# Kernel optimization log

Hardware: AMD Instinct MI355X
Metric: run time of the kernel (lower is better)

The kernel has to match this reference:

```python
import jax, jax.numpy as jnp
import numpy as np

DIM = 1024
NUM_HEADS = 16
DIM_PER_HEAD = 64
INNER = NUM_HEADS * DIM_PER_HEAD  # 1024
SCALE = DIM_PER_HEAD ** -0.5
EPS = 1e-10


def setup_inputs() -> dict:
    key = jax.random.key(0)
    k_x, k_m, k_qkv, k_wo, k_bo = jax.random.split(key, 5)
    b, l = 2, 2048
    x = jax.random.normal(k_x, (b, l, DIM), dtype=jnp.float32)
    # binary multiplicative mask [b, l, l]
    mask = jax.random.randint(k_m, (b, l, l), 0, 2).astype(jnp.float32)
    # nn.Linear(dim, 3*inner, bias=False): weight [3*inner, dim]; we store transposed [dim, 3*inner]
    W_qkv = jax.random.normal(k_qkv, (DIM, 3 * INNER), dtype=jnp.float32) * (DIM ** -0.5)
    W_out = jax.random.normal(k_wo, (INNER, DIM), dtype=jnp.float32) * (INNER ** -0.5)
    b_out = jax.random.normal(k_bo, (DIM,), dtype=jnp.float32) * 0.01
    return {"x": x, "mask": mask, "W_qkv": W_qkv, "W_out": W_out, "b_out": b_out}


def reference(x, mask, W_qkv, W_out, b_out):
    b, l, d = x.shape
    qkv = x @ W_qkv  # [b, l, 3*inner]
    qkv = qkv.reshape(b, l, 3, NUM_HEADS, DIM_PER_HEAD)
    qkv = jnp.transpose(qkv, (2, 0, 3, 1, 4))  # [3, b, h, l, dh]
    q, k, v = qkv[0], qkv[1], qkv[2]
    # softmax FIRST (no additive mask), matching the original module
    attn = jax.nn.softmax(jnp.einsum('bhid,bhjd->bhij', q, k) * SCALE, axis=-1)  # [b,h,l,l]
    # multiplicative mask then renormalize
    attn = attn * mask[:, None, :, :]
    attn = attn / (jnp.sum(attn, axis=-1, keepdims=True) + EPS)
    z = jnp.einsum('bhij,bhjd->bhid', attn, v)  # [b,h,l,dh]
    z = jnp.transpose(z, (0, 2, 1, 3)).reshape(b, l, INNER)
    out = z @ W_out + b_out  # dropout p=0 -> identity
    return out
```

## Files before the change

kernel.cpp:

```cpp
#include <hip/hip_runtime.h>
#include <hip/hip_bf16.h>

#define BATCH 2
#define SEQ   2048
#define DIM   1024
#define HEADS 16
#define DH    64
#define N_QKV 3072
#define M_TOT 4096
#define SCALE 0.125f
#define EPS   1e-10f
#define LOG2E 1.442695041f

typedef __attribute__((ext_vector_type(8))) _Float16 half8;
typedef __attribute__((ext_vector_type(4))) float f32x4;

static __device__ __forceinline__ unsigned short f2h(float f) {
    _Float16 h = (_Float16)f;
    return __builtin_bit_cast(unsigned short, h);
}
static __device__ __forceinline__ unsigned int pkrtz(float a, float b) {
#if defined(__has_builtin) && __has_builtin(__builtin_amdgcn_cvt_pkrtz)
    return __builtin_bit_cast(unsigned int, __builtin_amdgcn_cvt_pkrtz(a, b));
#else
    return (unsigned int)f2h(a) | ((unsigned int)f2h(b) << 16);
#endif
}
static __device__ __forceinline__ void glds16(const void* g, void* l) {
    __builtin_amdgcn_global_load_lds((const __attribute__((address_space(1))) void*)g,
                                     (__attribute__((address_space(3))) void*)l,
                                     16, 0, 0);
}

__global__ __launch_bounds__(256) void prepass(const float* __restrict__ x,
                                               unsigned short* __restrict__ xh,
                                               const float* __restrict__ Wq,
                                               unsigned short* __restrict__ WqT,
                                               const float* __restrict__ Wo,
                                               unsigned short* __restrict__ WoT,
                                               const float* __restrict__ mask,
                                               unsigned short* __restrict__ mbits) {
    const int bid = blockIdx.x;
    const int t   = threadIdx.x;
    __shared__ float tile[32][33];
    __shared__ unsigned char flags[16][256];

    if (bid < 4096) {
        const int i = bid * 256 + t;
        float4 v = reinterpret_cast<const float4*>(x)[i];
        uint2 o;
        o.x = pkrtz(v.x, v.y);
        o.y = pkrtz(v.z, v.w);
        reinterpret_cast<uint2*>(xh)[i] = o;
    } else if (bid < 8192) {
        const float* src; unsigned short* th; int rows, cols, bx;
        if (bid < 7168) { src = Wq; th = WqT; rows = 1024; cols = 3072; bx = bid - 4096;
        } else          { src = Wo; th = WoT; rows = 1024; cols = 1024; bx = bid - 7168; }
        const int nbx = cols / 32;
        const int c0 = (bx % nbx) * 32, r0 = (bx / nbx) * 32;
        const int tx = t & 31, ty = t >> 5;
        #pragma unroll
        for (int i = ty; i < 32; i += 8)
            tile[i][tx] = src[(long)(r0 + i) * cols + c0 + tx];
        __syncthreads();
        #pragma unroll
        for (int i = ty; i < 32; i += 8)
            th[(long)(c0 + i) * rows + r0 + tx] = f2h(tile[tx][i]);
    } else {
        const int bx = bid - 8192;
        const int it = bx & 127;
        const int bb = bx >> 7;
        const int R0 = it * 16;
        const int tl = t >> 6, ln = t & 63;
        for (int c0 = 0; c0 < SEQ; c0 += 256) {
            #pragma unroll
            for (int rr = 0; rr < 16; ++rr)
                flags[rr][t] = mask[((long)bb * SEQ + R0 + rr) * SEQ + c0 + t] != 0.f;
            __syncthreads();
            unsigned int bits = 0;
            #pragma unroll
            for (int nt = 0; nt < 4; ++nt)
                #pragma unroll
                for (int r = 0; r < 4; ++r)
                    bits |= (unsigned int)flags[ln & 15][tl * 64 + nt * 16 + ((ln >> 4) << 2) + r]
                            << (nt * 4 + r);
            mbits[(((long)bb * 128 + it) * 32 + (c0 >> 6) + tl) * 64 + ln] = (unsigned short)bits;
            __syncthreads();
        }
    }
}

__global__ __launch_bounds__(256, 3) void gemm_qkv_f16(
    const unsigned short* __restrict__ Ahg, const unsigned short* __restrict__ Bhg,
    unsigned short* __restrict__ qb, unsigned short* __restrict__ kb,
    unsigned short* __restrict__ vtb) {
    __shared__ __align__(16) unsigned short As[128 * 64];
    __shared__ __align__(16) unsigned short Bs[128 * 64];

    const int n0   = blockIdx.x * 128;
    const int m0   = blockIdx.y * 128;
    const int wave = threadIdx.x >> 6;
    const int lane = threadIdx.x & 63;
    const int l16  = lane & 15;
    const int g    = lane >> 4;
    const int wm   = wave & 1;
    const int wn   = wave >> 1;
    const int sw   = l16 & 7;

    const int sr8 = lane >> 3;
    const int scg = (lane & 7) ^ sr8;

    f32x4 acc[4][4] = {};

    for (int k0 = 0; k0 < DIM; k0 += 64) {
        #pragma unroll
        for (int i = 0; i < 4; ++i) {
            const int row = wave * 32 + i * 8;
            glds16(Ahg + (long)(m0 + row + sr8) * DIM + k0 + scg * 8, &As[row * 64]);
            glds16(Bhg + (long)(n0 + row + sr8) * DIM + k0 + scg * 8, &Bs[row * 64]);
        }
        __syncthreads();

        #pragma unroll
        for (int kc = 0; kc < 2; ++kc) {
            half8 a[4], b[4];
            #pragma unroll
            for (int mt = 0; mt < 4; ++mt)
                a[mt] = *reinterpret_cast<const half8*>(
                    &As[(wm * 64 + mt * 16 + l16) * 64 + (((kc * 4 + g) ^ sw) * 8)]);
            #pragma unroll
            for (int nt = 0; nt < 4; ++nt)
                b[nt] = *reinterpret_cast<const half8*>(
                    &Bs[(wn * 64 + nt * 16 + l16) * 64 + (((kc * 4 + g) ^ sw) * 8)]);
            #pragma unroll
            for (int mt = 0; mt < 4; ++mt)
                #pragma unroll
                for (int nt = 0; nt < 4; ++nt)
                    acc[mt][nt] = __builtin_amdgcn_mfma_f32_16x16x32_f16(
                        a[mt], b[nt], acc[mt][nt], 0, 0, 0);
        }
        __syncthreads();
    }

    #pragma unroll
    for (int nt = 0; nt < 4; ++nt) {
        const int n     = n0 + wn * 64 + nt * 16 + l16;
        const int which = n >> 10;
        const int rem   = n & 1023;
        const int head  = rem >> 6;
        const int d     = rem & 63;
        #pragma unroll
        for (int mt = 0; mt < 4; ++mt) {
            #pragma unroll
            for (int r = 0; r < 4; ++r) {
                const int m  = m0 + wm * 64 + mt * 16 + g * 4 + r;
                const int bb = m >> 11;
                const int li = m & 2047;
                const int bh_i = bb * HEADS + head;
                const float val = acc[mt][nt][r];
                if (which == 0)
                    qb[((long)bh_i * SEQ + li) * DH + d] = f2h(val * (SCALE * LOG2E));
                else if (which == 1)
                    kb[((long)bh_i * SEQ + li) * DH + d] = f2h(val);
                else
                    vtb[((long)bh_i * DH + d) * SEQ + li] = f2h(val);
            }
        }
    }
}

__global__ __launch_bounds__(256, 4) void gemm_out_f16(
    const unsigned short* __restrict__ Ahg, const unsigned short* __restrict__ Bhg,
    const float* __restrict__ bias, float* __restrict__ out) {
    __shared__ __align__(16) unsigned short As[64 * 64];
    __shared__ __align__(16) unsigned short Bs[64 * 64];

    const int n0   = blockIdx.x * 64;
    const int m0   = blockIdx.y * 64;
    const int wave = threadIdx.x >> 6;
    const int lane = threadIdx.x & 63;
    const int l16  = lane & 15;
    const int g    = lane >> 4;
    const int wm   = wave & 1;
    const int wn   = wave >> 1;
    const int sw   = l16 & 7;

    const int sr8 = lane >> 3;
    const int scg = (lane & 7) ^ sr8;

    f32x4 acc[2][2] = {};

    for (int k0 = 0; k0 < DIM; k0 += 64) {
        #pragma unroll
        for (int i = 0; i < 2; ++i) {
            const int row = wave * 16 + i * 8;
            glds16(Ahg + (long)(m0 + row + sr8) * DIM + k0 + scg * 8, &As[row * 64]);
            glds16(Bhg + (long)(n0 + row + sr8) * DIM + k0 + scg * 8, &Bs[row * 64]);
        }
        __syncthreads();

        half8 a[2][2];
        #pragma unroll
        for (int mt = 0; mt < 2; ++mt) {
            const int rbase = (wm * 32 + mt * 16 + l16) * 64;
            #pragma unroll
            for (int kc = 0; kc < 2; ++kc)
                a[mt][kc] = *reinterpret_cast<const half8*>(
                    &As[rbase + (((kc * 4 + g) ^ sw) * 8)]);
        }
        #pragma unroll
        for (int nt = 0; nt < 2; ++nt) {
            const int rbase = (wn * 32 + nt * 16 + l16) * 64;
            const half8 b0 = *reinterpret_cast<const half8*>(&Bs[rbase + (((0 + g) ^ sw) * 8)]);
            const half8 b1 = *reinterpret_cast<const half8*>(&Bs[rbase + (((4 + g) ^ sw) * 8)]);
            #pragma unroll
            for (int mt = 0; mt < 2; ++mt) {
                acc[mt][nt] = __builtin_amdgcn_mfma_f32_16x16x32_f16(a[mt][0], b0, acc[mt][nt], 0, 0, 0);
                acc[mt][nt] = __builtin_amdgcn_mfma_f32_16x16x32_f16(a[mt][1], b1, acc[mt][nt], 0, 0, 0);
            }
        }
        __syncthreads();
    }

    #pragma unroll
    for (int nt = 0; nt < 2; ++nt) {
        const int n  = n0 + wn * 32 + nt * 16 + l16;
        const float bv = bias[n];
        #pragma unroll
        for (int mt = 0; mt < 2; ++mt) {
            #pragma unroll
            for (int r = 0; r < 4; ++r) {
                const int m = m0 + wm * 32 + mt * 16 + g * 4 + r;
                out[(long)m * DIM + n] = acc[mt][nt][r] + bv;
            }
        }
    }
}

__global__ __launch_bounds__(512, 4) void attn_mfma(const unsigned short* __restrict__ qb,
                                                    const unsigned short* __restrict__ kb,
                                                    const unsigned short* __restrict__ vtb,
                                                    const unsigned short* __restrict__ mbits,
                                                    unsigned short* __restrict__ zh) {
    const int qt   = blockIdx.x;
    const int h    = blockIdx.y;
    const int bb   = blockIdx.z;
    const int bh   = bb * HEADS + h;
    const int wave = threadIdx.x >> 6;
    const int lane = threadIdx.x & 63;
    const int l16  = lane & 15;
    const int g    = lane >> 4;
    const int wm   = wave >> 1;
    const int wj   = wave & 1;

    const int myrow0 = qt * 128 + wm * 32;

    __shared__ __align__(16) unsigned short shm[32768];

    const int sr8 = lane >> 3;
    const int scg = (lane & 7) ^ sr8;
    const int sw  = l16 & 7;

    unsigned short* Ks = &shm[wj * 8192];
    unsigned short* Vs = &shm[wj * 8192 + 4096];
    unsigned short* P0 = &shm[16384 + wave * 1024];
    unsigned short* P1 = &shm[24576 + wave * 1024];

    const unsigned short* qptr = qb + ((long)bh * SEQ + myrow0 + l16) * DH + g * 8;
    const half8 q0 = *reinterpret_cast<const half8*>(qptr);
    const half8 q1 = *reinterpret_cast<const half8*>(qptr + 32);
    const half8 q2 = *reinterpret_cast<const half8*>(qptr + 16 * DH);
    const half8 q3 = *reinterpret_cast<const half8*>(qptr + 16 * DH + 32);

    half8 ones;
    #pragma unroll
    for (int j = 0; j < 8; ++j) ones[j] = (_Float16)1.0f;

    f32x4 o0[4] = {}, o1[4] = {};
    f32x4 oz0 = {0.f, 0.f, 0.f, 0.f};
    f32x4 oz1 = {0.f, 0.f, 0.f, 0.f};

    const unsigned short* mb =
        mbits + (((long)bb * 128 + qt * 8 + wm * 2) * 32 + wj * 16) * 64 + lane;
    const long kbase = (long)bh * SEQ * DH;
    const long vbase = (long)bh * DH * SEQ;
    const int  jb    = wj * 1024;

    for (int it = 0; it < 16; ++it) {
        const int j0 = jb + it * 64;
        const unsigned int bits0 = mb[(long)it * 64];
        const unsigned int bits1 = mb[(long)it * 64 + 2048];

        #pragma unroll
        for (int i = 0; i < 2; ++i) {
            const int row = wm * 16 + i * 8;
            glds16(kb  + kbase + (long)(j0 + row + sr8) * DH + scg * 8, Ks + row * 64);
            glds16(vtb + vbase + (long)(row + sr8) * SEQ + j0 + scg * 8, Vs + row * 64);
        }
        __syncthreads();

        #pragma unroll
        for (int nt = 0; nt < 4; ++nt) {
            const int rbase = (nt * 16 + l16) * 64;
            const half8 k0 = *reinterpret_cast<const half8*>(&Ks[rbase + ((0 + g) ^ sw) * 8]);
            const half8 k1 = *reinterpret_cast<const half8*>(&Ks[rbase + (((4 + g) ^ sw) * 8)]);
            f32x4 s0 = {0.f, 0.f, 0.f, 0.f};
            f32x4 s1 = {0.f, 0.f, 0.f, 0.f};
            s0 = __builtin_amdgcn_mfma_f32_16x16x32_f16(k0, q0, s0, 0, 0, 0);
            s0 = __builtin_amdgcn_mfma_f32_16x16x32_f16(k1, q1, s0, 0, 0, 0);
            s1 = __builtin_amdgcn_mfma_f32_16x16x32_f16(k0, q2, s1, 0, 0, 0);
            s1 = __builtin_amdgcn_mfma_f32_16x16x32_f16(k1, q3, s1, 0, 0, 0);

            float pa[4], pb[4];
            #pragma unroll
            for (int r = 0; r < 4; ++r) {
                const float e0 = __builtin_amdgcn_exp2f(s0[r]);
                const float e1 = __builtin_amdgcn_exp2f(s1[r]);
                pa[r] = ((bits0 >> (nt * 4 + r)) & 1u) ? e0 : 0.f;
                pb[r] = ((bits1 >> (nt * 4 + r)) & 1u) ? e1 : 0.f;
            }
            const int poff = l16 * 64 + (((2 * nt + (g >> 1)) ^ sw) * 8) + (g & 1) * 4;
            uint2 pk0, pk1;
            pk0.x = pkrtz(pa[0], pa[1]);
            pk0.y = pkrtz(pa[2], pa[3]);
            pk1.x = pkrtz(pb[0], pb[1]);
            pk1.y = pkrtz(pb[2], pb[3]);
            *reinterpret_cast<uint2*>(&P0[poff]) = pk0;
            *reinterpret_cast<uint2*>(&P1[poff]) = pk1;
        }

        const half8 pb00 = *reinterpret_cast<const half8*>(&P0[l16 * 64 + ((0 + g) ^ sw) * 8]);
        const half8 pb01 = *reinterpret_cast<const half8*>(&P0[l16 * 64 + (((4 + g) ^ sw) * 8)]);
        const half8 pb10 = *reinterpret_cast<const half8*>(&P1[l16 * 64 + ((0 + g) ^ sw) * 8]);
        const half8 pb11 = *reinterpret_cast<const half8*>(&P1[l16 * 64 + (((4 + g) ^ sw) * 8)]);

        #pragma unroll
        for (int dt = 0; dt < 4; ++dt) {
            const int vb = (dt * 16 + l16) * 64;
            const half8 v0 = *reinterpret_cast<const half8*>(&Vs[vb + ((0 + g) ^ sw) * 8]);
            const half8 v1 = *reinterpret_cast<const half8*>(&Vs[vb + (((4 + g) ^ sw) * 8)]);
            o0[dt] = __builtin_amdgcn_mfma_f32_16x16x32_f16(v0, pb00, o0[dt], 0, 0, 0);
            o0[dt] = __builtin_amdgcn_mfma_f32_16x16x32_f16(v1, pb01, o0[dt], 0, 0, 0);
            o1[dt] = __builtin_amdgcn_mfma_f32_16x16x32_f16(v0, pb10, o1[dt], 0, 0, 0);
            o1[dt] = __builtin_amdgcn_mfma_f32_16x16x32_f16(v1, pb11, o1[dt], 0, 0, 0);
        }
        oz0 = __builtin_amdgcn_mfma_f32_16x16x32_f16(ones, pb00, oz0, 0, 0, 0);
        oz0 = __builtin_amdgcn_mfma_f32_16x16x32_f16(ones, pb01, oz0, 0, 0, 0);
        oz1 = __builtin_amdgcn_mfma_f32_16x16x32_f16(ones, pb10, oz1, 0, 0, 0);
        oz1 = __builtin_amdgcn_mfma_f32_16x16x32_f16(ones, pb11, oz1, 0, 0, 0);
        __syncthreads();
    }

    float* cmb = (float*)shm;
    const int ZOFF = 128 * 68;
    const int ci0  = wm * 32 + l16;
    const int ci1  = ci0 + 16;
    if (wj == 1) {
        #pragma unroll
        for (int dt = 0; dt < 4; ++dt) {
            *reinterpret_cast<f32x4*>(&cmb[ci0 * 68 + dt * 16 + g * 4]) = o0[dt];
            *reinterpret_cast<f32x4*>(&cmb[ci1 * 68 + dt * 16 + g * 4]) = o1[dt];
        }
        if (g == 0) {
            cmb[ZOFF + ci0] = oz0[0];
            cmb[ZOFF + ci1] = oz1[0];
        }
    }
    __syncthreads();
    if (wj == 0) {
        const float Z0   = oz0[0] + cmb[ZOFF + ci0];
        const float Z1   = oz1[0] + cmb[ZOFF + ci1];
        const float inv0 = 1.f / (Z0 + 1e-30f);
        const float inv1 = 1.f / (Z1 + 1e-30f);
        const long obase0 = ((long)bb * SEQ + myrow0 + l16) * DIM + h * DH;
        const long obase1 = obase0 + (long)16 * DIM;
        #pragma unroll
        for (int dt = 0; dt < 4; ++dt) {
            const f32x4 oc0 = *reinterpret_cast<const f32x4*>(&cmb[ci0 * 68 + dt * 16 + g * 4]);
            const f32x4 oc1 = *reinterpret_cast<const f32x4*>(&cmb[ci1 * 68 + dt * 16 + g * 4]);
            uint2 pk;
            pk.x = pkrtz((o0[dt][0] + oc0[0]) * inv0, (o0[dt][1] + oc0[1]) * inv0);
            pk.y = pkrtz((o0[dt][2] + oc0[2]) * inv0, (o0[dt][3] + oc0[3]) * inv0);
            *reinterpret_cast<uint2*>(zh + obase0 + dt * 16 + g * 4) = pk;
            pk.x = pkrtz((o1[dt][0] + oc1[0]) * inv1, (o1[dt][1] + oc1[1]) * inv1);
            pk.y = pkrtz((o1[dt][2] + oc1[2]) * inv1, (o1[dt][3] + oc1[3]) * inv1);
            *reinterpret_cast<uint2*>(zh + obase1 + dt * 16 + g * 4) = pk;
        }
    }
}

extern "C" void kernel_launch(void* const* d_in, const int* in_sizes, int n_in,
                              void* d_out, int out_size, void* d_ws, size_t ws_size,
                              hipStream_t stream) {
    const float* x     = (const float*)d_in[0];
    const float* mask  = (const float*)d_in[1];
    const float* W_qkv = (const float*)d_in[2];
    const float* W_out = (const float*)d_in[3];
    const float* b_out = (const float*)d_in[4];
    float* out = (float*)d_out;

    unsigned short* ws = (unsigned short*)d_ws;
    unsigned short* xh    = ws;
    unsigned short* WqT   = xh    + 4194304;
    unsigned short* WoT   = WqT   + 3145728;
    unsigned short* qbu   = WoT   + 1048576;
    unsigned short* kbu   = qbu   + 4194304;
    unsigned short* vtb   = kbu   + 4194304;
    unsigned short* mbits = vtb   + 4194304;
    unsigned short* zz    = xh;

    prepass<<<8448, 256, 0, stream>>>(x, xh, W_qkv, WqT, W_out, WoT, mask, mbits);

    gemm_qkv_f16<<<dim3(24, 32), 256, 0, stream>>>(xh, WqT, qbu, kbu, vtb);

    attn_mfma<<<dim3(SEQ / 128, HEADS, BATCH), 512, 0, stream>>>(qbu, kbu, vtb, mbits, zz);

    gemm_out_f16<<<dim3(16, 64), 256, 0, stream>>>(zz, WoT, b_out, out);
}
```

Baseline: 229.9 us.

## Halve attention block to 64 query rows with XCD-aware flat grid and shared P buffer

```diff
diff --git a/kernel.cpp b/kernel.cpp
--- a/kernel.cpp
+++ b/kernel.cpp
@@ -237,14 +237,18 @@
     }
 }
 
-__global__ __launch_bounds__(512, 4) void attn_mfma(const unsigned short* __restrict__ qb,
+__global__ __launch_bounds__(256, 4) void attn_mfma(const unsigned short* __restrict__ qb,
                                                     const unsigned short* __restrict__ kb,
                                                     const unsigned short* __restrict__ vtb,
                                                     const unsigned short* __restrict__ mbits,
                                                     unsigned short* __restrict__ zh) {
-    const int qt   = blockIdx.x;
-    const int h    = blockIdx.y;
-    const int bb   = blockIdx.z;
+    const int flat = blockIdx.x;
+    const int xcd  = flat & 7;
+    const int rr   = flat >> 3;
+    const int hh   = xcd + 8 * (rr >> 5);
+    const int qt   = rr & 31;
+    const int h    = hh & 15;
+    const int bb   = hh >> 4;
     const int bh   = bb * HEADS + h;
     const int wave = threadIdx.x >> 6;
     const int lane = threadIdx.x & 63;
@@ -253,18 +257,16 @@
     const int wm   = wave >> 1;
     const int wj   = wave & 1;
 
-    const int myrow0 = qt * 128 + wm * 32;
-
-    __shared__ __align__(16) unsigned short shm[32768];
+    const int myrow0 = qt * 64 + wm * 32;
+
+    __shared__ __align__(16) unsigned short shm[20480];
+    unsigned short* Ks = &shm[wj * 8192];
+    unsigned short* Vs = &shm[wj * 8192 + 4096];
+    unsigned short* Pw = &shm[16384 + wave * 1024];
 
     const int sr8 = lane >> 3;
     const int scg = (lane & 7) ^ sr8;
     const int sw  = l16 & 7;
-
-    unsigned short* Ks = &shm[wj * 8192];
-    unsigned short* Vs = &shm[wj * 8192 + 4096];
-    unsigned short* P0 = &shm[16384 + wave * 1024];
-    unsigned short* P1 = &shm[24576 + wave * 1024];
 
     const unsigned short* qptr = qb + ((long)bh * SEQ + myrow0 + l16) * DH + g * 8;
     const half8 q0 = *reinterpret_cast<const half8*>(qptr);
@@ -281,24 +283,24 @@
     f32x4 oz1 = {0.f, 0.f, 0.f, 0.f};
 
     const unsigned short* mb =
-        mbits + (((long)bb * 128 + qt * 8 + wm * 2) * 32 + wj * 16) * 64 + lane;
+        mbits + (((long)bb * 128 + qt * 4 + wm * 2) * 32 + wj * 16) * 64 + lane;
     const long kbase = (long)bh * SEQ * DH;
     const long vbase = (long)bh * DH * SEQ;
-    const int  jb    = wj * 1024;
 
     for (int it = 0; it < 16; ++it) {
-        const int j0 = jb + it * 64;
+        const int j0 = wj * 1024 + it * 64;
         const unsigned int bits0 = mb[(long)it * 64];
         const unsigned int bits1 = mb[(long)it * 64 + 2048];
 
         #pragma unroll
-        for (int i = 0; i < 2; ++i) {
-            const int row = wm * 16 + i * 8;
+        for (int i = 0; i < 4; ++i) {
+            const int row = wm * 32 + i * 8;
             glds16(kb  + kbase + (long)(j0 + row + sr8) * DH + scg * 8, Ks + row * 64);
             glds16(vtb + vbase + (long)(row + sr8) * SEQ + j0 + scg * 8, Vs + row * 64);
         }
         __syncthreads();
 
+        uint2 p1s[4];
         #pragma unroll
         for (int nt = 0; nt < 4; ++nt) {
             const int rbase = (nt * 16 + l16) * 64;
@@ -320,19 +322,23 @@
                 pb[r] = ((bits1 >> (nt * 4 + r)) & 1u) ? e1 : 0.f;
             }
             const int poff = l16 * 64 + (((2 * nt + (g >> 1)) ^ sw) * 8) + (g & 1) * 4;
-            uint2 pk0, pk1;
+            uint2 pk0;
             pk0.x = pkrtz(pa[0], pa[1]);
             pk0.y = pkrtz(pa[2], pa[3]);
-            pk1.x = pkrtz(pb[0], pb[1]);
-            pk1.y = pkrtz(pb[2], pb[3]);
-            *reinterpret_cast<uint2*>(&P0[poff]) = pk0;
-            *reinterpret_cast<uint2*>(&P1[poff]) = pk1;
-        }
-
-        const half8 pb00 = *reinterpret_cast<const half8*>(&P0[l16 * 64 + ((0 + g) ^ sw) * 8]);
-        const half8 pb01 = *reinterpret_cast<const half8*>(&P0[l16 * 64 + (((4 + g) ^ sw) * 8)]);
-        const half8 pb10 = *reinterpret_cast<const half8*>(&P1[l16 * 64 + ((0 + g) ^ sw) * 8]);
-        const half8 pb11 = *reinterpret_cast<const half8*>(&P1[l16 * 64 + (((4 + g) ^ sw) * 8)]);
+            *reinterpret_cast<uint2*>(&Pw[poff]) = pk0;
+            p1s[nt].x = pkrtz(pb[0], pb[1]);
+            p1s[nt].y = pkrtz(pb[2], pb[3]);
+        }
+
+        const half8 pb00 = *reinterpret_cast<const half8*>(&Pw[l16 * 64 + ((0 + g) ^ sw) * 8]);
+        const half8 pb01 = *reinterpret_cast<const half8*>(&Pw[l16 * 64 + (((4 + g) ^ sw) * 8)]);
+        #pragma unroll
+        for (int nt = 0; nt < 4; ++nt) {
+            const int poff = l16 * 64 + (((2 * nt + (g >> 1)) ^ sw) * 8) + (g & 1) * 4;
+            *reinterpret_cast<uint2*>(&Pw[poff]) = p1s[nt];
+        }
+        const half8 pb10 = *reinterpret_cast<const half8*>(&Pw[l16 * 64 + ((0 + g) ^ sw) * 8]);
+        const half8 pb11 = *reinterpret_cast<const half8*>(&Pw[l16 * 64 + (((4 + g) ^ sw) * 8)]);
 
         #pragma unroll
         for (int dt = 0; dt < 4; ++dt) {
@@ -352,7 +358,7 @@
     }
 
     float* cmb = (float*)shm;
-    const int ZOFF = 128 * 68;
+    const int ZOFF = 64 * 68;
     const int ci0  = wm * 32 + l16;
     const int ci1  = ci0 + 16;
     if (wj == 1) {
@@ -413,7 +419,7 @@
 
     gemm_qkv_f16<<<dim3(24, 32), 256, 0, stream>>>(xh, WqT, qbu, kbu, vtb);
 
-    attn_mfma<<<dim3(SEQ / 128, HEADS, BATCH), 512, 0, stream>>>(qbu, kbu, vtb, mbits, zz);
+    attn_mfma<<<1024, 256, 0, stream>>>(qbu, kbu, vtb, mbits, zz);
 
     gemm_out_f16<<<dim3(16, 64), 256, 0, stream>>>(zz, WoT, b_out, out);
 }
```

Result: slower. 239.5 us (+4.1%).
